# Optimization experiments

Hardware: AMD Instinct MI355X
Metric: run time of the kernel (lower is better)

## Reference

```python
import jax, jax.numpy as jnp
import numpy as np

N = 20000; E = 120000; D = 1024; H = 8; C = D // H; L = 2; EPS = 1e-5


def setup_inputs() -> dict:
    key = jax.random.key(0)
    ks = jax.random.split(key, 12)
    s = 0.03  # init scale (glorot-ish for d=1024)
    return {
        'x': jax.random.normal(ks[0], (N, D), jnp.float32),
        'edge_index': jax.random.randint(ks[1], (2, E), 0, N),
        'edge_attr': jax.random.randint(ks[2], (E,), 0, 5),
        'node_types': jax.random.randint(ks[3], (N,), 0, 6),
        'node_type_emb': jax.random.normal(ks[4], (6, D), jnp.float32) * s,
        'edge_type_emb': jax.random.normal(ks[5], (5, D), jnp.float32) * s,
        'W_l': jax.random.normal(ks[6], (L, D, D), jnp.float32) * s,
        'b_l': jnp.zeros((L, D), jnp.float32),
        'W_r': jax.random.normal(ks[7], (L, D, D), jnp.float32) * s,
        'b_r': jnp.zeros((L, D), jnp.float32),
        'W_e': jax.random.normal(ks[8], (L, D, D), jnp.float32) * s,
        'att': jax.random.normal(ks[9], (L, H, C), jnp.float32) * s,
        'bias': jnp.zeros((L, D), jnp.float32),
        'ln_gamma': jnp.ones((L, D), jnp.float32),
        'ln_beta': jnp.zeros((L, D), jnp.float32),
        'W_out': jax.random.normal(ks[10], (D, D), jnp.float32) * s,
        'b_out': jnp.zeros((D,), jnp.float32),
        'gate': jnp.array([0.5], jnp.float32),
    }


def _layer_norm(y, g, b):
    mu = y.mean(-1, keepdims=True)
    var = ((y - mu) ** 2).mean(-1, keepdims=True)
    return (y - mu) * jax.lax.rsqrt(var + EPS) * g + b


def reference(x, edge_index, edge_attr, node_types, node_type_emb, edge_type_emb,
              W_l, b_l, W_r, b_r, W_e, att, bias, ln_gamma, ln_beta,
              W_out, b_out, gate):
    src, dst = edge_index[0], edge_index[1]
    e_emb = edge_type_emb[edge_attr]                       # [E, D]
    # PyG add_self_loops(fill_value='mean'): self-loop edge attr = mean of
    # incoming edge attrs (0 if no incoming edges)
    deg = jax.ops.segment_sum(jnp.ones((E,), x.dtype), dst, num_segments=N)
    loop_e = jax.ops.segment_sum(e_emb, dst, num_segments=N) / jnp.maximum(deg, 1.0)[:, None]
    idx = jnp.arange(N, dtype=src.dtype)
    src_a = jnp.concatenate([src, idx])                    # [E+N]
    dst_a = jnp.concatenate([dst, idx])
    e_all = jnp.concatenate([e_emb, loop_e], axis=0)       # [E+N, D]

    h = x + node_type_emb[node_types]
    for l in range(L):
        xl = (h @ W_l[l] + b_l[l]).reshape(N, H, C)        # lin_l (source)
        xr = (h @ W_r[l] + b_r[l]).reshape(N, H, C)        # lin_r (target)
        ee = (e_all @ W_e[l]).reshape(-1, H, C)            # lin_edge (no bias)
        s = jax.nn.leaky_relu(xl[src_a] + xr[dst_a] + ee, 0.2)
        logits = jnp.einsum('ehc,hc->eh', s, att[l])       # [E+N, H]
        # segment softmax over incoming edges per target node
        mx = jax.ops.segment_max(logits, dst_a, num_segments=N)
        ex = jnp.exp(logits - mx[dst_a])
        den = jax.ops.segment_sum(ex, dst_a, num_segments=N)
        alpha = ex / den[dst_a]                            # [E+N, H]
        out = jax.ops.segment_sum(xl[src_a] * alpha[..., None], dst_a,
                                  num_segments=N).reshape(N, D) + bias[l]
        h2 = jax.nn.elu(out)                               # dropout is identity in eval
        h = _layer_norm(h2 + h, ln_gamma[l], ln_beta[l])
    return x + gate * (h @ W_out + b_out)
```

## Files before the change

kernel.cpp:

```cpp
#include <hip/hip_runtime.h>


#define NN 20000
#define NE 120000
#define DD 1024
#define NH 8

typedef __attribute__((ext_vector_type(4))) float f32x4;
typedef __bf16 bf16x8 __attribute__((ext_vector_type(8)));

__device__ __forceinline__ unsigned short f2bf(float f) {
  unsigned int u = __float_as_uint(f);
  u += 0x7FFFu + ((u >> 16) & 1u);
  return (unsigned short)(u >> 16);
}
__device__ __forceinline__ float bf2f(unsigned short u) {
  return __uint_as_float((unsigned int)u << 16);
}
__device__ __forceinline__ void unpack8(uint4 u, float* f) {
  f[0] = __uint_as_float(u.x << 16); f[1] = __uint_as_float(u.x & 0xFFFF0000u);
  f[2] = __uint_as_float(u.y << 16); f[3] = __uint_as_float(u.y & 0xFFFF0000u);
  f[4] = __uint_as_float(u.z << 16); f[5] = __uint_as_float(u.z & 0xFFFF0000u);
  f[6] = __uint_as_float(u.w << 16); f[7] = __uint_as_float(u.w & 0xFFFF0000u);
}
__device__ __forceinline__ void unpack4(uint2 u, float* f) {
  f[0] = __uint_as_float(u.x << 16); f[1] = __uint_as_float(u.x & 0xFFFF0000u);
  f[2] = __uint_as_float(u.y << 16); f[3] = __uint_as_float(u.y & 0xFFFF0000u);
}


__global__ __launch_bounds__(256) void count_kernel(
    const int* __restrict__ EI, const int* __restrict__ eattr, int* __restrict__ cnt) {
  int e = blockIdx.x * 256 + threadIdx.x;
  if (e < NE) {
    int d = EI[NE + e];
    int t = eattr[e];
    atomicAdd(&cnt[d * 5 + t], 1);
  }
}

__global__ __launch_bounds__(1024) void scan_kernel(
    const int* __restrict__ cnt, int* __restrict__ rowptr, int* __restrict__ cursor) {
  __shared__ int wsum[16];
  __shared__ int carry_s;
  int tid = threadIdx.x, lane = tid & 63, wv = tid >> 6;
  if (tid == 0) carry_s = 0;
  __syncthreads();
  for (int base = 0; base < NN; base += 1024) {
    int n = base + tid;
    int d = 0;
    if (n < NN) {
      const int* c = cnt + n * 5;
      d = c[0] + c[1] + c[2] + c[3] + c[4];
    }
    int v = d;
    #pragma unroll
    for (int off = 1; off < 64; off <<= 1) {
      int t = __shfl_up(v, off);
      if (lane >= off) v += t;
    }
    if (lane == 63) wsum[wv] = v;
    __syncthreads();
    int woff = 0;
    #pragma unroll
    for (int w = 0; w < 16; ++w) if (w < wv) woff += wsum[w];
    int carry = carry_s;
    int excl = carry + woff + v - d;
    if (n < NN) { rowptr[n] = excl; cursor[n] = excl; }
    __syncthreads();
    if (tid == 0) {
      int t = 0;
      #pragma unroll
      for (int w = 0; w < 16; ++w) t += wsum[w];
      carry_s = carry + t;
    }
    __syncthreads();
  }
  if (tid == 0) rowptr[NN] = carry_s;
}

__global__ __launch_bounds__(256) void scatter_kernel(
    const int* __restrict__ EI, const int* __restrict__ eattr,
    int* __restrict__ cursor, int* __restrict__ epk) {
  int e = blockIdx.x * 256 + threadIdx.x;
  if (e < NE) {
    int d = EI[NE + e];
    int s = EI[e];
    int t = eattr[e];
    int pos = atomicAdd(&cursor[d], 1);
    epk[pos] = (s << 3) | t;
  }
}


__global__ __launch_bounds__(256) void init_h_kernel(
    const float* __restrict__ x, const int* __restrict__ ntypes,
    const float* __restrict__ ntemb, float* __restrict__ h,
    unsigned short* __restrict__ hb) {
  int idx = blockIdx.x * 256 + threadIdx.x;
  int n = idx >> 8;
  int d4 = idx & 255;
  int t = ntypes[n];
  float4 xv = ((const float4*)x)[idx];
  float4 ev = ((const float4*)ntemb)[t * 256 + d4];
  float4 o;
  o.x = xv.x + ev.x; o.y = xv.y + ev.y; o.z = xv.z + ev.z; o.w = xv.w + ev.w;
  ((float4*)h)[idx] = o;
  ushort4 hv;
  hv.x = f2bf(o.x); hv.y = f2bf(o.y); hv.z = f2bf(o.z); hv.w = f2bf(o.w);
  ((ushort4*)hb)[idx] = hv;
}


__global__ __launch_bounds__(256) void transpose_w_kernel(
    const float* __restrict__ W, unsigned short* __restrict__ WT) {
  __shared__ float tile[32][33];
  int tx = threadIdx.x & 31, ty = threadIdx.x >> 5;
  int bx = blockIdx.x * 32;
  int by = blockIdx.y * 32;
  #pragma unroll
  for (int r = 0; r < 4; ++r)
    tile[ty + r * 8][tx] = W[(size_t)(by + ty + r * 8) * DD + bx + tx];
  __syncthreads();
  #pragma unroll
  for (int r = 0; r < 4; ++r)
    WT[(size_t)(bx + ty + r * 8) * DD + by + tx] = f2bf(tile[tx][ty + r * 8]);
}


__global__ __launch_bounds__(256) void m_kernel(
    const float* __restrict__ ete, const float* __restrict__ We, float* __restrict__ M) {
  __shared__ float red[4][5][64];
  const int jl = threadIdx.x & 63;
  const int kc = threadIdx.x >> 6;
  const int j = blockIdx.x * 64 + jl;
  float acc[5] = {0.f, 0.f, 0.f, 0.f, 0.f};
  const int k0 = kc * 256;
  for (int k = k0; k < k0 + 256; ++k) {
    float w = We[(size_t)k * DD + j];
    #pragma unroll
    for (int t = 0; t < 5; ++t) acc[t] += ete[t * DD + k] * w;
  }
  #pragma unroll
  for (int t = 0; t < 5; ++t) red[kc][t][jl] = acc[t];
  __syncthreads();
  if (threadIdx.x < 64) {
    #pragma unroll
    for (int t = 0; t < 5; ++t)
      M[t * DD + blockIdx.x * 64 + threadIdx.x] =
          red[0][t][threadIdx.x] + red[1][t][threadIdx.x] +
          red[2][t][threadIdx.x] + red[3][t][threadIdx.x];
  }
}


__global__ __launch_bounds__(256) void gemm_bf16(
    const unsigned short* __restrict__ A, const unsigned short* __restrict__ BT,
    const float* __restrict__ bias0, const float* __restrict__ bias1,
    void* __restrict__ C0v, void* __restrict__ C1v,
    const float* __restrict__ resid, const float* __restrict__ gatep,
    int M, int mode) {
  __shared__ unsigned short lsA[128 * 32];
  __shared__ unsigned short lsB[128 * 32];
  const int tid = threadIdx.x;
  const int lane = tid & 63;
  const int wv = tid >> 6;
  const int wm = wv & 1, wn = wv >> 1;

  const int nwg = gridDim.x * gridDim.y;
  const int lid = blockIdx.y * gridDim.x + blockIdx.x;
  const int cpx = nwg >> 3;
  const int swz = (lid & 7) * cpx + (lid >> 3);
  const int bm = swz / gridDim.x, bn = swz % gridDim.x;

  const int row0 = bm * 128, col0 = bn * 128;
  const int l15 = lane & 15, quad = lane >> 4;

  f32x4 acc[4][4];
  #pragma unroll
  for (int mt = 0; mt < 4; ++mt)
    #pragma unroll
    for (int nt = 0; nt < 4; ++nt) {
      f32x4 z = {0.f, 0.f, 0.f, 0.f};
      acc[mt][nt] = z;
    }

  const int r_in = lane >> 2;
  const int kchunk = (lane & 3) * 8;

  for (int kk = 0; kk < DD; kk += 32) {
    #pragma unroll
    for (int j = 0; j < 2; ++j) {
      int r = wv * 32 + j * 16;
      int gr = row0 + r + r_in;
      if (gr > M - 1) gr = M - 1;
      const unsigned short* gpA = A + (size_t)gr * DD + kk + kchunk;
      __builtin_amdgcn_global_load_lds(
          (const __attribute__((address_space(1))) unsigned int*)gpA,
          (__attribute__((address_space(3))) unsigned int*)(lsA + r * 32), 16, 0, 0);
      const unsigned short* gpB = BT + (size_t)(col0 + r + r_in) * DD + kk + kchunk;
      __builtin_amdgcn_global_load_lds(
          (const __attribute__((address_space(1))) unsigned int*)gpB,
          (__attribute__((address_space(3))) unsigned int*)(lsB + r * 32), 16, 0, 0);
    }
    __syncthreads();
    bf16x8 af[4], bfr[4];
    #pragma unroll
    for (int mt = 0; mt < 4; ++mt)
      af[mt] = *(const bf16x8*)(lsA + (wm * 64 + mt * 16 + l15) * 32 + quad * 8);
    #pragma unroll
    for (int nt = 0; nt < 4; ++nt)
      bfr[nt] = *(const bf16x8*)(lsB + (wn * 64 + nt * 16 + l15) * 32 + quad * 8);
    #pragma unroll
    for (int mt = 0; mt < 4; ++mt)
      #pragma unroll
      for (int nt = 0; nt < 4; ++nt)
        acc[mt][nt] = __builtin_amdgcn_mfma_f32_16x16x32_bf16(af[mt], bfr[nt], acc[mt][nt], 0, 0, 0);
    __syncthreads();
  }

  if (mode == 0) {
    unsigned short* Cb = (unsigned short*)(bn < 8 ? C0v : C1v);
    const float* bp = (bn < 8) ? bias0 : bias1;
    int coff = (bn < 8) ? 0 : 1024;
    #pragma unroll
    for (int mt = 0; mt < 4; ++mt) {
      #pragma unroll
      for (int r = 0; r < 4; ++r) {
        int grow = row0 + wm * 64 + mt * 16 + quad * 4 + r;
        if (grow >= M) continue;
        #pragma unroll
        for (int nt = 0; nt < 4; ++nt) {
          int c = col0 - coff + wn * 64 + nt * 16 + l15;
          Cb[(size_t)grow * DD + c] = f2bf(acc[mt][nt][r] + bp[c]);
        }
      }
    }
  } else {
    float* Cp = (float*)C0v;
    float g = gatep[0];
    #pragma unroll
    for (int mt = 0; mt < 4; ++mt) {
      #pragma unroll
      for (int r = 0; r < 4; ++r) {
        int grow = row0 + wm * 64 + mt * 16 + quad * 4 + r;
        if (grow >= M) continue;
        #pragma unroll
        for (int nt = 0; nt < 4; ++nt) {
          int c = col0 + wn * 64 + nt * 16 + l15;
          float v = acc[mt][nt][r] + bias0[c];
          Cp[(size_t)grow * DD + c] = resid[(size_t)grow * DD + c] + g * v;
        }
      }
    }
  }
}


__global__ __launch_bounds__(256) void attn_kernel(
    const unsigned short* __restrict__ xlb, const unsigned short* __restrict__ xrb,
    const int* __restrict__ rowptr, const int* __restrict__ epk,
    const int* __restrict__ cnt, const float* __restrict__ Mbuf,
    const float* __restrict__ attl, const float* __restrict__ biasl,
    const float* __restrict__ gammal, const float* __restrict__ betal,
    float* __restrict__ h, unsigned short* __restrict__ hb, int write_h) {
  __shared__ float red1[4], red2[4];
  const int lane = threadIdx.x & 63;
  const int wv = threadIdx.x >> 6;
  const int n = blockIdx.x;
  const int ch = wv * 256 + lane * 4;

  const int beg = rowptr[n], end = rowptr[n + 1];
  const int* c5 = cnt + n * 5;
  int c0 = c5[0], c1 = c5[1], c2 = c5[2], c3 = c5[3], c4 = c5[4];

  float xrf[4], attf[4];
  {
    uint2 a = *(const uint2*)(xrb + (size_t)n * DD + ch);
    unpack4(a, xrf);
    float4 t = *(const float4*)(attl + ch);
    attf[0] = t.x; attf[1] = t.y; attf[2] = t.z; attf[3] = t.w;
  }
  float acc0 = 0.f, acc1 = 0.f, acc2 = 0.f, acc3 = 0.f;
  float den = 0.f;

  for (int base = beg; base < end; base += 64) {
    int cc = min(64, end - base);
    int packed = 0;
    if (lane < cc) packed = epk[base + lane];
    for (int j = 0; j < cc; ++j) {
      int pk = __shfl(packed, j);
      int src = pk >> 3, at = pk & 7;
      uint2 v = *(const uint2*)(xlb + (size_t)src * DD + ch);
      float4 m = *(const float4*)(Mbuf + at * DD + ch);
      float vf[4];
      unpack4(v, vf);
      float s0 = vf[0] + xrf[0] + m.x; s0 = fmaxf(s0, 0.2f * s0);
      float s1 = vf[1] + xrf[1] + m.y; s1 = fmaxf(s1, 0.2f * s1);
      float s2 = vf[2] + xrf[2] + m.z; s2 = fmaxf(s2, 0.2f * s2);
      float s3 = vf[3] + xrf[3] + m.w; s3 = fmaxf(s3, 0.2f * s3);
      float lg = s0 * attf[0] + s1 * attf[1] + s2 * attf[2] + s3 * attf[3];
      lg += __shfl_xor(lg, 1);
      lg += __shfl_xor(lg, 2);
      lg += __shfl_xor(lg, 4);
      lg += __shfl_xor(lg, 8);
      lg += __shfl_xor(lg, 16);
      float p = __expf(lg);
      den += p;
      acc0 += p * vf[0]; acc1 += p * vf[1];
      acc2 += p * vf[2]; acc3 += p * vf[3];
    }
  }

  {
    float inv = 1.f / fmaxf((float)(c0 + c1 + c2 + c3 + c4), 1.f);
    float w0 = c0 * inv, w1 = c1 * inv, w2 = c2 * inv, w3 = c3 * inv, w4 = c4 * inv;
    uint2 v = *(const uint2*)(xlb + (size_t)n * DD + ch);
    float vf[4];
    unpack4(v, vf);
    float4 m0 = *(const float4*)(Mbuf + 0 * DD + ch);
    float4 m1 = *(const float4*)(Mbuf + 1 * DD + ch);
    float4 m2 = *(const float4*)(Mbuf + 2 * DD + ch);
    float4 m3 = *(const float4*)(Mbuf + 3 * DD + ch);
    float4 m4 = *(const float4*)(Mbuf + 4 * DD + ch);
    float e0 = w0 * m0.x + w1 * m1.x + w2 * m2.x + w3 * m3.x + w4 * m4.x;
    float e1 = w0 * m0.y + w1 * m1.y + w2 * m2.y + w3 * m3.y + w4 * m4.y;
    float e2 = w0 * m0.z + w1 * m1.z + w2 * m2.z + w3 * m3.z + w4 * m4.z;
    float e3 = w0 * m0.w + w1 * m1.w + w2 * m2.w + w3 * m3.w + w4 * m4.w;
    float s0 = vf[0] + xrf[0] + e0; s0 = fmaxf(s0, 0.2f * s0);
    float s1 = vf[1] + xrf[1] + e1; s1 = fmaxf(s1, 0.2f * s1);
    float s2 = vf[2] + xrf[2] + e2; s2 = fmaxf(s2, 0.2f * s2);
    float s3 = vf[3] + xrf[3] + e3; s3 = fmaxf(s3, 0.2f * s3);
    float lg = s0 * attf[0] + s1 * attf[1] + s2 * attf[2] + s3 * attf[3];
    lg += __shfl_xor(lg, 1);
    lg += __shfl_xor(lg, 2);
    lg += __shfl_xor(lg, 4);
    lg += __shfl_xor(lg, 8);
    lg += __shfl_xor(lg, 16);
    float p = __expf(lg);
    den += p;
    acc0 += p * vf[0]; acc1 += p * vf[1];
    acc2 += p * vf[2]; acc3 += p * vf[3];
  }

  float invd = 1.f / den;
  float4 b4 = *(const float4*)(biasl + ch);
  float4 h4 = *(const float4*)(h + (size_t)n * DD + ch);
  float o0 = acc0 * invd + b4.x;
  float o1 = acc1 * invd + b4.y;
  float o2 = acc2 * invd + b4.z;
  float o3 = acc3 * invd + b4.w;
  o0 = o0 > 0.f ? o0 : (__expf(o0) - 1.f);
  o1 = o1 > 0.f ? o1 : (__expf(o1) - 1.f);
  o2 = o2 > 0.f ? o2 : (__expf(o2) - 1.f);
  o3 = o3 > 0.f ? o3 : (__expf(o3) - 1.f);
  float y0 = o0 + h4.x, y1 = o1 + h4.y, y2 = o2 + h4.z, y3 = o3 + h4.w;
  float s1r = y0 + y1 + y2 + y3;
  float s2r = y0 * y0 + y1 * y1 + y2 * y2 + y3 * y3;
  #pragma unroll
  for (int off = 1; off < 64; off <<= 1) {
    s1r += __shfl_xor(s1r, off);
    s2r += __shfl_xor(s2r, off);
  }
  if (lane == 0) { red1[wv] = s1r; red2[wv] = s2r; }
  __syncthreads();
  float t1 = red1[0] + red1[1] + red1[2] + red1[3];
  float t2 = red2[0] + red2[1] + red2[2] + red2[3];
  float mu = t1 * (1.f / 1024.f);
  float var = t2 * (1.f / 1024.f) - mu * mu;
  float rs = rsqrtf(var + 1e-5f);
  {
    float4 g4 = *(const float4*)(gammal + ch);
    float4 be4 = *(const float4*)(betal + ch);
    float w0 = (y0 - mu) * rs * g4.x + be4.x;
    float w1 = (y1 - mu) * rs * g4.y + be4.y;
    float w2 = (y2 - mu) * rs * g4.z + be4.z;
    float w3 = (y3 - mu) * rs * g4.w + be4.w;
    if (write_h) {
      float4 o4; o4.x = w0; o4.y = w1; o4.z = w2; o4.w = w3;
      *(float4*)(h + (size_t)n * DD + ch) = o4;
    }
    uint2 pk;
    pk.x = (unsigned int)f2bf(w0) | ((unsigned int)f2bf(w1) << 16);
    pk.y = (unsigned int)f2bf(w2) | ((unsigned int)f2bf(w3) << 16);
    *(uint2*)(hb + (size_t)n * DD + ch) = pk;
  }
}


extern "C" void kernel_launch(void* const* d_in, const int* in_sizes, int n_in,
                              void* d_out, int out_size, void* d_ws, size_t ws_size,
                              hipStream_t stream) {
  (void)in_sizes; (void)n_in; (void)out_size; (void)ws_size;
  const float* x      = (const float*)d_in[0];
  const int*   EI     = (const int*)d_in[1];
  const int*   eattr  = (const int*)d_in[2];
  const int*   ntypes = (const int*)d_in[3];
  const float* ntemb  = (const float*)d_in[4];
  const float* etemb  = (const float*)d_in[5];
  const float* W_l    = (const float*)d_in[6];
  const float* b_l    = (const float*)d_in[7];
  const float* W_r    = (const float*)d_in[8];
  const float* b_r    = (const float*)d_in[9];
  const float* W_e    = (const float*)d_in[10];
  const float* att    = (const float*)d_in[11];
  const float* bias   = (const float*)d_in[12];
  const float* gamma  = (const float*)d_in[13];
  const float* beta   = (const float*)d_in[14];
  const float* W_out  = (const float*)d_in[15];
  const float* b_out  = (const float*)d_in[16];
  const float* gate   = (const float*)d_in[17];
  float* out = (float*)d_out;

  char* ws = (char*)d_ws;
  size_t off = 0;
  auto alloc = [&](size_t bytes) {
    char* p = ws + off;
    off = (off + bytes + 255) & ~(size_t)255;
    return p;
  };
  float*          h       = (float*)alloc((size_t)NN * DD * 4);
  unsigned short* hb      = (unsigned short*)alloc((size_t)NN * DD * 2);
  unsigned short* xlb     = (unsigned short*)alloc((size_t)NN * DD * 2);
  unsigned short* xrb     = (unsigned short*)alloc((size_t)NN * DD * 2);
  unsigned short* WTcat   = (unsigned short*)alloc((size_t)2 * DD * DD * 2);
  unsigned short* WT2     = (unsigned short*)alloc((size_t)DD * DD * 2);
  float*          Mbuf    = (float*)alloc((size_t)5 * DD * 4);
  int*            countb  = (int*)alloc((size_t)NN * 5 * 4);
  int*            rowptr  = (int*)alloc((size_t)(NN + 1) * 4);
  int*            cursor  = (int*)alloc((size_t)NN * 4);
  int*            epk     = (int*)alloc((size_t)NE * 4);

  hipMemsetAsync(countb, 0, (size_t)NN * 5 * 4, stream);
  count_kernel<<<(NE + 255) / 256, 256, 0, stream>>>(EI, eattr, countb);
  scan_kernel<<<1, 1024, 0, stream>>>(countb, rowptr, cursor);
  scatter_kernel<<<(NE + 255) / 256, 256, 0, stream>>>(EI, eattr, cursor, epk);
  init_h_kernel<<<NN, 256, 0, stream>>>(x, ntypes, ntemb, h, hb);

  dim3 tgrid(DD / 32, DD / 32);
  dim3 ggrid2(16, (NN + 127) / 128);
  dim3 ggrid1(8, (NN + 127) / 128);
  for (int l = 0; l < 2; ++l) {
    transpose_w_kernel<<<tgrid, 256, 0, stream>>>(W_l + (size_t)l * DD * DD, WTcat);
    transpose_w_kernel<<<tgrid, 256, 0, stream>>>(W_r + (size_t)l * DD * DD, WTcat + (size_t)DD * DD);
    m_kernel<<<DD / 64, 256, 0, stream>>>(etemb, W_e + (size_t)l * DD * DD, Mbuf);
    gemm_bf16<<<ggrid2, 256, 0, stream>>>(hb, WTcat, b_l + l * DD, b_r + l * DD,
                                          xlb, xrb, nullptr, nullptr, NN, 0);
    attn_kernel<<<NN, 256, 0, stream>>>(xlb, xrb, rowptr, epk, countb, Mbuf,
                                        att + l * DD, bias + l * DD,
                                        gamma + l * DD, beta + l * DD, h, hb,
                                        l == 0 ? 1 : 0);
  }
  transpose_w_kernel<<<tgrid, 256, 0, stream>>>(W_out, WT2);
  gemm_bf16<<<ggrid1, 256, 0, stream>>>(hb, WT2, b_out, nullptr,
                                        out, nullptr, x, gate, NN, 1);
}
```

Baseline: 809.8 us.

## Replace 128x128 bf16 GEMM with double-buffered 256x256 tile kernel using swizzled LDS

```diff
diff --git a/kernel.cpp b/kernel.cpp
--- a/kernel.cpp
+++ b/kernel.cpp
@@ -13,15 +13,6 @@
   unsigned int u = __float_as_uint(f);
   u += 0x7FFFu + ((u >> 16) & 1u);
   return (unsigned short)(u >> 16);
-}
-__device__ __forceinline__ float bf2f(unsigned short u) {
-  return __uint_as_float((unsigned int)u << 16);
-}
-__device__ __forceinline__ void unpack8(uint4 u, float* f) {
-  f[0] = __uint_as_float(u.x << 16); f[1] = __uint_as_float(u.x & 0xFFFF0000u);
-  f[2] = __uint_as_float(u.y << 16); f[3] = __uint_as_float(u.y & 0xFFFF0000u);
-  f[4] = __uint_as_float(u.z << 16); f[5] = __uint_as_float(u.z & 0xFFFF0000u);
-  f[6] = __uint_as_float(u.w << 16); f[7] = __uint_as_float(u.w & 0xFFFF0000u);
 }
 __device__ __forceinline__ void unpack4(uint2 u, float* f) {
   f[0] = __uint_as_float(u.x << 16); f[1] = __uint_as_float(u.x & 0xFFFF0000u);
@@ -154,102 +145,161 @@
 }
 
 
-__global__ __launch_bounds__(256) void gemm_bf16(
+__global__ __launch_bounds__(512, 2) void gemm256(
     const unsigned short* __restrict__ A, const unsigned short* __restrict__ BT,
     const float* __restrict__ bias0, const float* __restrict__ bias1,
     void* __restrict__ C0v, void* __restrict__ C1v,
     const float* __restrict__ resid, const float* __restrict__ gatep,
     int M, int mode) {
-  __shared__ unsigned short lsA[128 * 32];
-  __shared__ unsigned short lsB[128 * 32];
+  extern __shared__ char smem[];
   const int tid = threadIdx.x;
   const int lane = tid & 63;
   const int wv = tid >> 6;
-  const int wm = wv & 1, wn = wv >> 1;
+  const int wm = wv >> 2;
+  const int wn = wv & 3;
+  const int l15 = lane & 15, quad = lane >> 4;
 
   const int nwg = gridDim.x * gridDim.y;
   const int lid = blockIdx.y * gridDim.x + blockIdx.x;
-  const int cpx = nwg >> 3;
-  const int swz = (lid & 7) * cpx + (lid >> 3);
+  const int q8 = nwg >> 3, r8 = nwg & 7;
+  const int xcd = lid & 7, ixq = lid >> 3;
+  const int swz = (xcd < r8 ? xcd * (q8 + 1) : r8 * (q8 + 1) + (xcd - r8) * q8) + ixq;
   const int bm = swz / gridDim.x, bn = swz % gridDim.x;
-
-  const int row0 = bm * 128, col0 = bn * 128;
-  const int l15 = lane & 15, quad = lane >> 4;
-
-  f32x4 acc[4][4];
+  const int row0 = bm * 256, col0 = bn * 256;
+
+  const int lr = lane >> 3;
+  const int sb = lane & 7;
+  const int xb = (lane >> 5) & 1;
+  const int rxor = (((lane >> 2) & 1) << 1) | ((lane >> 3) & 1);
+
+  f32x4 acc[8][4];
   #pragma unroll
-  for (int mt = 0; mt < 4; ++mt)
+  for (int mt = 0; mt < 8; ++mt)
     #pragma unroll
     for (int nt = 0; nt < 4; ++nt) {
       f32x4 z = {0.f, 0.f, 0.f, 0.f};
       acc[mt][nt] = z;
     }
-
-  const int r_in = lane >> 2;
-  const int kchunk = (lane & 3) * 8;
-
-  for (int kk = 0; kk < DD; kk += 32) {
-    #pragma unroll
-    for (int j = 0; j < 2; ++j) {
-      int r = wv * 32 + j * 16;
-      int gr = row0 + r + r_in;
-      if (gr > M - 1) gr = M - 1;
-      const unsigned short* gpA = A + (size_t)gr * DD + kk + kchunk;
-      __builtin_amdgcn_global_load_lds(
-          (const __attribute__((address_space(1))) unsigned int*)gpA,
-          (__attribute__((address_space(3))) unsigned int*)(lsA + r * 32), 16, 0, 0);
-      const unsigned short* gpB = BT + (size_t)(col0 + r + r_in) * DD + kk + kchunk;
-      __builtin_amdgcn_global_load_lds(
-          (const __attribute__((address_space(1))) unsigned int*)gpB,
-          (__attribute__((address_space(3))) unsigned int*)(lsB + r * 32), 16, 0, 0);
-    }
-    __syncthreads();
-    bf16x8 af[4], bfr[4];
+  bf16x8 aF[4][2];
+  bf16x8 bF[2][2][2];
+
+  auto stage = [&](int kt, int db) {
+    char* base = smem + db * 65536;
+    #pragma unroll
+    for (int h = 0; h < 2; ++h) {
+      #pragma unroll
+      for (int i = 0; i < 2; ++i) {
+        const int bi = wv * 2 + i;
+        const int rloc = h * 128 + bi * 8 + lr;
+        const int csl = ((sb ^ (xb << 1) ^ i) << 3);
+        int ra = row0 + rloc; if (ra > M - 1) ra = M - 1;
+        __builtin_amdgcn_global_load_lds(
+            (const __attribute__((address_space(1))) unsigned int*)(A + (size_t)ra * 1024 + kt * 64 + csl),
+            (__attribute__((address_space(3))) unsigned int*)(base + h * 16384 + bi * 1024), 16, 0, 0);
+        const int rb = col0 + rloc;
+        __builtin_amdgcn_global_load_lds(
+            (const __attribute__((address_space(1))) unsigned int*)(BT + (size_t)rb * 1024 + kt * 64 + csl),
+            (__attribute__((address_space(3))) unsigned int*)(base + 32768 + h * 16384 + bi * 1024), 16, 0, 0);
+      }
+    }
+  };
+  auto readA = [&](int db, int mh) {
+    const char* Ab = smem + db * 65536;
+    #pragma unroll
+    for (int mt = 0; mt < 4; ++mt) {
+      const int rl = wm * 128 + mh * 64 + mt * 16 + l15;
+      #pragma unroll
+      for (int kk = 0; kk < 2; ++kk) {
+        const int sp = (kk * 4 + quad) ^ rxor;
+        aF[mt][kk] = *(const bf16x8*)(Ab + rl * 128 + sp * 16);
+      }
+    }
+  };
+  auto readB = [&](int db, int nh) {
+    const char* Bb = smem + db * 65536 + 32768;
+    #pragma unroll
+    for (int nt = 0; nt < 2; ++nt) {
+      const int rl = wn * 64 + nh * 32 + nt * 16 + l15;
+      #pragma unroll
+      for (int kk = 0; kk < 2; ++kk) {
+        const int sp = (kk * 4 + quad) ^ rxor;
+        bF[nh][nt][kk] = *(const bf16x8*)(Bb + rl * 128 + sp * 16);
+      }
+    }
+  };
+  auto mfmaQ = [&](int a, int b) {
+    __builtin_amdgcn_s_setprio(1);
     #pragma unroll
     for (int mt = 0; mt < 4; ++mt)
-      af[mt] = *(const bf16x8*)(lsA + (wm * 64 + mt * 16 + l15) * 32 + quad * 8);
-    #pragma unroll
-    for (int nt = 0; nt < 4; ++nt)
-      bfr[nt] = *(const bf16x8*)(lsB + (wn * 64 + nt * 16 + l15) * 32 + quad * 8);
-    #pragma unroll
-    for (int mt = 0; mt < 4; ++mt)
-      #pragma unroll
-      for (int nt = 0; nt < 4; ++nt)
-        acc[mt][nt] = __builtin_amdgcn_mfma_f32_16x16x32_bf16(af[mt], bfr[nt], acc[mt][nt], 0, 0, 0);
-    __syncthreads();
+      #pragma unroll
+      for (int nt = 0; nt < 2; ++nt)
+        #pragma unroll
+        for (int kk = 0; kk < 2; ++kk)
+          acc[a * 4 + mt][b * 2 + nt] = __builtin_amdgcn_mfma_f32_16x16x32_bf16(
+              aF[mt][kk], bF[b][nt][kk], acc[a * 4 + mt][b * 2 + nt], 0, 0, 0);
+    __builtin_amdgcn_s_setprio(0);
+  };
+
+#define SBAR() { __builtin_amdgcn_s_barrier(); asm volatile("" ::: "memory"); }
+
+  stage(0, 0);
+  asm volatile("s_waitcnt vmcnt(0)" ::: "memory");
+  SBAR();
+
+  for (int kt = 0; kt < 16; ++kt) {
+    const int cb = kt & 1;
+    readA(cb, 0);
+    readB(cb, 0);
+    if (kt < 15) stage(kt + 1, cb ^ 1);
+    SBAR();
+    mfmaQ(0, 0);
+    SBAR();
+    readB(cb, 1);
+    SBAR();
+    mfmaQ(0, 1);
+    SBAR();
+    readA(cb, 1);
+    SBAR();
+    mfmaQ(1, 1);
+    SBAR();
+    asm volatile("s_waitcnt vmcnt(0)" ::: "memory");
+    SBAR();
+    mfmaQ(1, 0);
+    SBAR();
   }
 
   if (mode == 0) {
-    unsigned short* Cb = (unsigned short*)(bn < 8 ? C0v : C1v);
-    const float* bp = (bn < 8) ? bias0 : bias1;
-    int coff = (bn < 8) ? 0 : 1024;
-    #pragma unroll
-    for (int mt = 0; mt < 4; ++mt) {
+    #pragma unroll
+    for (int mt = 0; mt < 8; ++mt) {
       #pragma unroll
       for (int r = 0; r < 4; ++r) {
-        int grow = row0 + wm * 64 + mt * 16 + quad * 4 + r;
+        const int grow = row0 + wm * 128 + mt * 16 + quad * 4 + r;
         if (grow >= M) continue;
         #pragma unroll
         for (int nt = 0; nt < 4; ++nt) {
-          int c = col0 - coff + wn * 64 + nt * 16 + l15;
-          Cb[(size_t)grow * DD + c] = f2bf(acc[mt][nt][r] + bp[c]);
+          const int cg = col0 + wn * 64 + nt * 16 + l15;
+          const int half = cg >> 10;
+          const int cl = cg & 1023;
+          unsigned short* Cb = (unsigned short*)(half ? C1v : C0v);
+          const float* bp = half ? bias1 : bias0;
+          Cb[(size_t)grow * 1024 + cl] = f2bf(acc[mt][nt][r] + bp[cl]);
         }
       }
     }
   } else {
     float* Cp = (float*)C0v;
-    float g = gatep[0];
-    #pragma unroll
-    for (int mt = 0; mt < 4; ++mt) {
+    const float g = gatep[0];
+    #pragma unroll
+    for (int mt = 0; mt < 8; ++mt) {
       #pragma unroll
       for (int r = 0; r < 4; ++r) {
-        int grow = row0 + wm * 64 + mt * 16 + quad * 4 + r;
+        const int grow = row0 + wm * 128 + mt * 16 + quad * 4 + r;
         if (grow >= M) continue;
         #pragma unroll
         for (int nt = 0; nt < 4; ++nt) {
-          int c = col0 + wn * 64 + nt * 16 + l15;
-          float v = acc[mt][nt][r] + bias0[c];
-          Cp[(size_t)grow * DD + c] = resid[(size_t)grow * DD + c] + g * v;
+          const int cg = col0 + wn * 64 + nt * 16 + l15;
+          float v = acc[mt][nt][r] + bias0[cg];
+          Cp[(size_t)grow * 1024 + cg] = resid[(size_t)grow * 1024 + cg] + g * v;
         }
       }
     }
@@ -431,6 +481,13 @@
   int*            cursor  = (int*)alloc((size_t)NN * 4);
   int*            epk     = (int*)alloc((size_t)NE * 4);
 
+  static bool attr_done = false;
+  if (!attr_done) {
+    (void)hipFuncSetAttribute((const void*)gemm256,
+                              hipFuncAttributeMaxDynamicSharedMemorySize, 131072);
+    attr_done = true;
+  }
+
   hipMemsetAsync(countb, 0, (size_t)NN * 5 * 4, stream);
   count_kernel<<<(NE + 255) / 256, 256, 0, stream>>>(EI, eattr, countb);
   scan_kernel<<<1, 1024, 0, stream>>>(countb, rowptr, cursor);
@@ -438,20 +495,20 @@
   init_h_kernel<<<NN, 256, 0, stream>>>(x, ntypes, ntemb, h, hb);
 
   dim3 tgrid(DD / 32, DD / 32);
-  dim3 ggrid2(16, (NN + 127) / 128);
-  dim3 ggrid1(8, (NN + 127) / 128);
+  dim3 g2(8, (NN + 255) / 256);
+  dim3 g1(4, (NN + 255) / 256);
   for (int l = 0; l < 2; ++l) {
     transpose_w_kernel<<<tgrid, 256, 0, stream>>>(W_l + (size_t)l * DD * DD, WTcat);
     transpose_w_kernel<<<tgrid, 256, 0, stream>>>(W_r + (size_t)l * DD * DD, WTcat + (size_t)DD * DD);
     m_kernel<<<DD / 64, 256, 0, stream>>>(etemb, W_e + (size_t)l * DD * DD, Mbuf);
-    gemm_bf16<<<ggrid2, 256, 0, stream>>>(hb, WTcat, b_l + l * DD, b_r + l * DD,
-                                          xlb, xrb, nullptr, nullptr, NN, 0);
+    gemm256<<<g2, 512, 131072, stream>>>(hb, WTcat, b_l + l * DD, b_r + l * DD,
+                                         xlb, xrb, nullptr, nullptr, NN, 0);
     attn_kernel<<<NN, 256, 0, stream>>>(xlb, xrb, rowptr, epk, countb, Mbuf,
                                         att + l * DD, bias + l * DD,
                                         gamma + l * DD, beta + l * DD, h, hb,
                                         l == 0 ? 1 : 0);
   }
   transpose_w_kernel<<<tgrid, 256, 0, stream>>>(W_out, WT2);
-  gemm_bf16<<<ggrid1, 256, 0, stream>>>(hb, WT2, b_out, nullptr,
-                                        out, nullptr, x, gate, NN, 1);
-}
+  gemm256<<<g1, 512, 131072, stream>>>(hb, WT2, b_out, nullptr,
+                                       out, nullptr, x, gate, NN, 1);
+}
```

Result: slower. 888.6 us (+9.7%).
